# Performance work log

Hardware: AMD Instinct MI355X
Metric: run time of the kernel (lower is better)

The kernel has to match this reference:

```python
import jax, jax.numpy as jnp
import numpy as np

T, B, V, H = 128, 32, 10000, 1024

def setup_inputs() -> dict:
    key = jax.random.key(0)
    ks = jax.random.split(key, 9)
    inp = {
        "inputs": jax.random.normal(ks[0], (T, B, V), dtype=jnp.float32),
        "H0": jnp.zeros((B, H), dtype=jnp.float32),
        "W_xz": jax.random.normal(ks[1], (V, H), dtype=jnp.float32) * 0.01,
        "W_hz": jax.random.normal(ks[2], (H, H), dtype=jnp.float32) * 0.01,
        "b_z": jnp.zeros((H,), dtype=jnp.float32),
        "W_xr": jax.random.normal(ks[3], (V, H), dtype=jnp.float32) * 0.01,
        "W_hr": jax.random.normal(ks[4], (H, H), dtype=jnp.float32) * 0.01,
        "b_r": jnp.zeros((H,), dtype=jnp.float32),
        "W_xh": jax.random.normal(ks[5], (V, H), dtype=jnp.float32) * 0.01,
        "W_hh": jax.random.normal(ks[6], (H, H), dtype=jnp.float32) * 0.01,
        "b_h": jnp.zeros((H,), dtype=jnp.float32),
        "W_hq": jax.random.normal(ks[7], (H, V), dtype=jnp.float32) * 0.01,
        "b_q": jnp.zeros((V,), dtype=jnp.float32),
    }
    return inp


def reference(inputs, H0, W_xz, W_hz, b_z, W_xr, W_hr, b_r, W_xh, W_hh, b_h, W_hq, b_q):
    # Batch all input-side projections across the whole sequence (same math,
    # just hoisted out of the recurrence): [T,B,V] @ [V,H] -> [T,B,H]
    Xz = jnp.einsum('tbv,vh->tbh', inputs, W_xz) + b_z
    Xr = jnp.einsum('tbv,vh->tbh', inputs, W_xr) + b_r
    Xh = jnp.einsum('tbv,vh->tbh', inputs, W_xh) + b_h

    def step(Hprev, xs):
        xz, xr, xh = xs
        Z = jax.nn.sigmoid(xz + Hprev @ W_hz)
        R = jax.nn.sigmoid(xr + Hprev @ W_hr)
        H_tilda = jnp.tanh(xh + (R * Hprev) @ W_hh)
        Hn = Z * Hprev + (1.0 - Z) * H_tilda
        return Hn, Hn

    H_last, Hs = jax.lax.scan(step, H0, (Xz, Xr, Xh))  # Hs: [T,B,H]
    outputs = jnp.einsum('tbh,hv->tbv', Hs, W_hq) + b_q  # [T,B,V]
    return outputs, H_last
```

## Files before the change

kernel.cpp:

```cpp
#include <hip/hip_runtime.h>
#include <cstdint>

typedef unsigned short u16;
typedef __attribute__((ext_vector_type(8))) short bf16x8;
typedef __attribute__((ext_vector_type(4))) float f32x4;
typedef __attribute__((ext_vector_type(4))) unsigned short u16x4;

#define AS_GLOBAL __attribute__((address_space(1)))
#define AS_LDS    __attribute__((address_space(3)))

__device__ __forceinline__ void gld_lds16(const void* g, void* l) {
    __builtin_amdgcn_global_load_lds((const AS_GLOBAL unsigned int*)g,
                                     (AS_LDS unsigned int*)l, 16, 0, 0);
}

__device__ __forceinline__ u16 f2bf(float f) {
    union { float f; unsigned int u; } v; v.f = f;
    unsigned int u = v.u;
    u = (u + 0x7FFFu + ((u >> 16) & 1u)) >> 16;
    return (u16)u;
}

__device__ __forceinline__ f32x4 mfma16(bf16x8 a, bf16x8 b, f32x4 c) {
    return __builtin_amdgcn_mfma_f32_16x16x32_bf16(a, b, c, 0, 0, 0);
}

__device__ __forceinline__ float sigm(float x) {
    return 1.f / (1.f + __expf(-x));
}

__global__ __launch_bounds__(256) void gemm_bt(
    const u16* __restrict__ A, const u16* __restrict__ BT,
    const float* __restrict__ bias, float* __restrict__ C,
    int M, int N, int K, int ldc, int Nstore)
{
    __shared__ u16 As[128 * 32];
    __shared__ u16 Bs[128 * 32];

    const int tid  = threadIdx.x;
    const int lane = tid & 63;
    const int wave = tid >> 6;
    const int quad = lane >> 4;
    const int l16  = lane & 15;
    const int m0 = blockIdx.y * 128;
    const int n0 = blockIdx.x * 128;
    const int wm = (wave >> 1) * 64;
    const int wn = (wave & 1) * 64;

    f32x4 acc[4][4];
#pragma unroll
    for (int i = 0; i < 4; i++)
#pragma unroll
        for (int j = 0; j < 4; j++) acc[i][j] = (f32x4){0.f, 0.f, 0.f, 0.f};

    const int s0 = tid, s1 = tid + 256;
    const int r0 = s0 >> 2, c0 = (s0 & 3) * 8;
    const int r1 = s1 >> 2, c1 = (s1 & 3) * 8;

    const u16* ga0 = A  + (size_t)(m0 + r0) * K + c0;
    const u16* ga1 = A  + (size_t)(m0 + r1) * K + c1;
    const u16* gb0 = BT + (size_t)(n0 + r0) * K + c0;
    const u16* gb1 = BT + (size_t)(n0 + r1) * K + c1;
    u16* la0 = &As[s0 * 8];
    u16* la1 = &As[s1 * 8];
    u16* lb0 = &Bs[s0 * 8];
    u16* lb1 = &Bs[s1 * 8];

    const u16* lra = &As[(wm + l16) * 32 + quad * 8];
    const u16* lrb = &Bs[(wn + l16) * 32 + quad * 8];

    const int nk = K >> 5;
    for (int kb = 0; kb < nk; ++kb) {
        const int k0 = kb << 5;
        gld_lds16(ga0 + k0, la0);
        gld_lds16(ga1 + k0, la1);
        gld_lds16(gb0 + k0, lb0);
        gld_lds16(gb1 + k0, lb1);
        __syncthreads();
        bf16x8 a[4], b[4];
#pragma unroll
        for (int i = 0; i < 4; i++) a[i] = *(const bf16x8*)(lra + i * 16 * 32);
#pragma unroll
        for (int j = 0; j < 4; j++) b[j] = *(const bf16x8*)(lrb + j * 16 * 32);
#pragma unroll
        for (int i = 0; i < 4; i++)
#pragma unroll
            for (int j = 0; j < 4; j++)
                acc[i][j] = mfma16(a[i], b[j], acc[i][j]);
        __syncthreads();
    }

#pragma unroll
    for (int i = 0; i < 4; i++) {
#pragma unroll
        for (int r = 0; r < 4; r++) {
            const int row = m0 + wm + i * 16 + quad * 4 + r;
#pragma unroll
            for (int j = 0; j < 4; j++) {
                const int col = n0 + wn + j * 16 + l16;
                if (col < Nstore)
                    C[(size_t)row * ldc + col] = acc[i][j][r] + bias[col];
            }
        }
    }
}

__global__ __launch_bounds__(256) void k_step1(
    const u16* __restrict__ Hbf, const float* __restrict__ Hf,
    const float* __restrict__ Xzr,
    const u16* __restrict__ WzrT,
    float* __restrict__ Zbuf, u16* __restrict__ RHbf)
{
    const int tid = threadIdx.x, lane = tid & 63, wave = tid >> 6;
    const int quad = lane >> 4, l16 = lane & 15;
    const int n0 = (blockIdx.x * 4 + wave) * 16;

    f32x4 acc0 = (f32x4){0,0,0,0}, acc1 = (f32x4){0,0,0,0};
    const u16* Arow0 = Hbf + l16 * 1024 + quad * 8;
    const u16* Arow1 = Hbf + (16 + l16) * 1024 + quad * 8;
    const u16* Brow  = WzrT + (size_t)(n0 + l16) * 1024 + quad * 8;
#pragma unroll 8
    for (int kb = 0; kb < 32; ++kb) {
        bf16x8 a0 = *(const bf16x8*)(Arow0 + kb * 32);
        bf16x8 a1 = *(const bf16x8*)(Arow1 + kb * 32);
        bf16x8 b  = *(const bf16x8*)(Brow + kb * 32);
        acc0 = mfma16(a0, b, acc0);
        acc1 = mfma16(a1, b, acc1);
    }
    const int n = n0 + l16;
#pragma unroll
    for (int r = 0; r < 4; r++) {
        const int b0 = quad * 4 + r;
        const int b1 = b0 + 16;
        float v0 = acc0[r] + Xzr[b0 * 3072 + n];
        float v1 = acc1[r] + Xzr[b1 * 3072 + n];
        if (n < 1024) {
            Zbuf[b0 * 1024 + n] = sigm(v0);
            Zbuf[b1 * 1024 + n] = sigm(v1);
        } else {
            const int m_ = n - 1024;
            RHbf[b0 * 1024 + m_] = f2bf(sigm(v0) * Hf[b0 * 1024 + m_]);
            RHbf[b1 * 1024 + m_] = f2bf(sigm(v1) * Hf[b1 * 1024 + m_]);
        }
    }
}

__global__ __launch_bounds__(256) void k_step2(
    const u16* __restrict__ RHbf, const u16* __restrict__ WhhT,
    const float* __restrict__ Xh,
    const float* __restrict__ Zbuf,
    float* __restrict__ Hf, u16* __restrict__ Hbf, u16* __restrict__ Hsbf_t)
{
    const int tid = threadIdx.x, lane = tid & 63, wave = tid >> 6;
    const int quad = lane >> 4, l16 = lane & 15;
    const int n0 = (blockIdx.x * 4 + wave) * 16;

    f32x4 acc0 = (f32x4){0,0,0,0}, acc1 = (f32x4){0,0,0,0};
    const u16* Arow0 = RHbf + l16 * 1024 + quad * 8;
    const u16* Arow1 = RHbf + (16 + l16) * 1024 + quad * 8;
    const u16* Brow  = WhhT + (size_t)(n0 + l16) * 1024 + quad * 8;
#pragma unroll 8
    for (int kb = 0; kb < 32; ++kb) {
        bf16x8 a0 = *(const bf16x8*)(Arow0 + kb * 32);
        bf16x8 a1 = *(const bf16x8*)(Arow1 + kb * 32);
        bf16x8 b  = *(const bf16x8*)(Brow + kb * 32);
        acc0 = mfma16(a0, b, acc0);
        acc1 = mfma16(a1, b, acc1);
    }
    const int n = n0 + l16;
#pragma unroll
    for (int r = 0; r < 4; r++) {
        const int b0 = quad * 4 + r;
        const int b1 = b0 + 16;
#pragma unroll
        for (int s = 0; s < 2; s++) {
            const int bb = s ? b1 : b0;
            float v = (s ? acc1[r] : acc0[r]) + Xh[bb * 3072 + n];
            float ht = tanhf(v);
            float z  = Zbuf[bb * 1024 + n];
            float hp = Hf[bb * 1024 + n];
            float hn = z * hp + (1.f - z) * ht;
            Hf[bb * 1024 + n] = hn;
            u16 hb = f2bf(hn);
            Hbf[bb * 1024 + n] = hb;
            Hsbf_t[bb * 1024 + n] = hb;
        }
    }
}

__global__ void k_cast_pad(const float* __restrict__ src, u16* __restrict__ dst,
                           int rows, int K0, int Kp)
{
    const size_t total = (size_t)rows * (size_t)(Kp >> 2);
    for (size_t idx = (size_t)blockIdx.x * blockDim.x + threadIdx.x;
         idx < total; idx += (size_t)gridDim.x * blockDim.x) {
        const int kq = (int)(idx % (size_t)(Kp >> 2));
        const int r  = (int)(idx / (size_t)(Kp >> 2));
        const int k  = kq << 2;
        u16x4 o;
        if (k + 3 < K0) {
            const float4 v = *(const float4*)(src + (size_t)r * K0 + k);
            o[0] = f2bf(v.x); o[1] = f2bf(v.y); o[2] = f2bf(v.z); o[3] = f2bf(v.w);
        } else {
#pragma unroll
            for (int i = 0; i < 4; i++)
                o[i] = (k + i < K0) ? f2bf(src[(size_t)r * K0 + k + i]) : (u16)0;
        }
        *(u16x4*)(dst + (size_t)r * Kp + k) = o;
    }
}

__global__ void k_transpose_cast(const float* __restrict__ src, u16* __restrict__ dst,
                                 int K0, int N0, int Kp, int rowOff)
{
    __shared__ float tile[32][33];
    const int kb = blockIdx.x * 32, nb = blockIdx.y * 32;
    const int tx = threadIdx.x, ty = threadIdx.y;
#pragma unroll
    for (int i = 0; i < 4; i++) {
        const int k = kb + ty + i * 8, n = nb + tx;
        tile[ty + i * 8][tx] = (k < K0 && n < N0) ? src[(size_t)k * N0 + n] : 0.f;
    }
    __syncthreads();
#pragma unroll
    for (int i = 0; i < 4; i++) {
        const int n = nb + ty + i * 8, k = kb + tx;
        dst[(size_t)(rowOff + n) * Kp + k] = f2bf(tile[tx][ty + i * 8]);
    }
}

__global__ void k_bias_cat(const float* __restrict__ bz, const float* __restrict__ br,
                           const float* __restrict__ bh, float* __restrict__ bcat)
{
    const int i = blockIdx.x * 256 + threadIdx.x;
    if (i < 1024) bcat[i] = bz[i];
    else if (i < 2048) bcat[i] = br[i - 1024];
    else if (i < 3072) bcat[i] = bh[i - 2048];
}

__global__ void k_h0(const float* __restrict__ H0, float* __restrict__ Hf,
                     u16* __restrict__ Hbf)
{
    const int i = blockIdx.x * 256 + threadIdx.x;
    if (i < 32 * 1024) { float v = H0[i]; Hf[i] = v; Hbf[i] = f2bf(v); }
}

extern "C" void kernel_launch(void* const* d_in, const int* in_sizes, int n_in,
                              void* d_out, int out_size, void* d_ws, size_t ws_size,
                              hipStream_t stream)
{
    const float* inputs = (const float*)d_in[0];
    const float* H0     = (const float*)d_in[1];
    const float* W_xz   = (const float*)d_in[2];
    const float* W_hz   = (const float*)d_in[3];
    const float* b_z    = (const float*)d_in[4];
    const float* W_xr   = (const float*)d_in[5];
    const float* W_hr   = (const float*)d_in[6];
    const float* b_r    = (const float*)d_in[7];
    const float* W_xh   = (const float*)d_in[8];
    const float* W_hh   = (const float*)d_in[9];
    const float* b_h    = (const float*)d_in[10];
    const float* W_hq   = (const float*)d_in[11];
    const float* b_q    = (const float*)d_in[12];
    float* out = (float*)d_out;

    constexpr int T = 128, B = 32, V = 10000, H = 1024;
    constexpr int Vp = 10016;
    constexpr int MB = T * B;
    constexpr int Np3 = 10112;

    char* p = (char*)d_ws;
    auto alloc = [&](size_t bytes) -> void* {
        void* q = (void*)p; p += (bytes + 255) & ~(size_t)255; return q;
    };
    u16*   Abf  = (u16*)  alloc((size_t)MB * Vp * 2);
    u16*   WxT  = (u16*)  alloc((size_t)3072 * Vp * 2);
    float* Xzrh = (float*)alloc((size_t)MB * 3072 * 4);
    u16*   Hsbf = (u16*)  alloc((size_t)MB * H * 2);
    u16*   WzrT = (u16*)  alloc((size_t)2048 * H * 2);
    u16*   WhhT = (u16*)  alloc((size_t)H * H * 2);
    u16*   WhqT = (u16*)  alloc((size_t)Np3 * H * 2);
    float* bcat = (float*)alloc(3072 * 4);
    float* Hf   = (float*)alloc((size_t)B * H * 4);
    u16*   Hbf  = (u16*)  alloc((size_t)B * H * 2);
    float* Zbuf = (float*)alloc((size_t)B * H * 4);
    u16*   RHbf = (u16*)  alloc((size_t)B * H * 2);

    {
        size_t total = (size_t)MB * (Vp / 4);
        int blocks = (int)((total + 255) / 256);
        k_cast_pad<<<blocks, 256, 0, stream>>>(inputs, Abf, MB, V, Vp);
    }
    dim3 tb(32, 8);
    k_transpose_cast<<<dim3(Vp / 32, H / 32), tb, 0, stream>>>(W_xz, WxT, V, H, Vp, 0);
    k_transpose_cast<<<dim3(Vp / 32, H / 32), tb, 0, stream>>>(W_xr, WxT, V, H, Vp, 1024);
    k_transpose_cast<<<dim3(Vp / 32, H / 32), tb, 0, stream>>>(W_xh, WxT, V, H, Vp, 2048);
    k_transpose_cast<<<dim3(H / 32, H / 32), tb, 0, stream>>>(W_hz, WzrT, H, H, H, 0);
    k_transpose_cast<<<dim3(H / 32, H / 32), tb, 0, stream>>>(W_hr, WzrT, H, H, H, 1024);
    k_transpose_cast<<<dim3(H / 32, H / 32), tb, 0, stream>>>(W_hh, WhhT, H, H, H, 0);
    k_transpose_cast<<<dim3(H / 32, Np3 / 32), tb, 0, stream>>>(W_hq, WhqT, H, V, H, 0);
    k_bias_cat<<<12, 256, 0, stream>>>(b_z, b_r, b_h, bcat);
    k_h0<<<128, 256, 0, stream>>>(H0, Hf, Hbf);

    gemm_bt<<<dim3(3072 / 128, MB / 128), 256, 0, stream>>>(
        Abf, WxT, bcat, Xzrh, MB, 3072, Vp, 3072, 3072);

    for (int t = 0; t < T; ++t) {
        k_step1<<<32, 256, 0, stream>>>(
            Hbf, Hf, Xzrh + (size_t)t * B * 3072, WzrT, Zbuf, RHbf);
        k_step2<<<16, 256, 0, stream>>>(
            RHbf, WhhT, Xzrh + (size_t)t * B * 3072 + 2048, Zbuf,
            Hf, Hbf, Hsbf + (size_t)t * B * H);
    }

    gemm_bt<<<dim3(Np3 / 128, MB / 128), 256, 0, stream>>>(
        Hsbf, WhqT, b_q, out, MB, Np3, H, V, V);

    hipMemcpyAsync(out + (size_t)MB * V, Hf, (size_t)B * H * 4,
                   hipMemcpyDeviceToDevice, stream);
}
```

Measured before the change: 4.999 ms.

## Fuse recurrence steps into one persistent cooperative kernel with LDS-resident weights

Replaces the 256 per-timestep kernel launches with a single cooperative kernel that loops over all timesteps, separating the gate phase and the candidate phase with grid-wide barriers. Each block loads its slice of the recurrent weight matrices into LDS once and reuses it across every step, avoiding repeated global/L2 weight reads. The second GEMM splits K across waves with an LDS reduction. The cost is two grid syncs per step, occupancy limited by the large LDS footprint, and reliance on cooperative launch residency.

New measurement: 4.482 ms. 10.3% less time.

```diff
diff --git a/kernel.cpp b/kernel.cpp
--- a/kernel.cpp
+++ b/kernel.cpp
@@ -1,5 +1,8 @@
 #include <hip/hip_runtime.h>
+#include <hip/hip_cooperative_groups.h>
 #include <cstdint>
+
+namespace cg = cooperative_groups;
 
 typedef unsigned short u16;
 typedef __attribute__((ext_vector_type(8))) short bf16x8;
@@ -105,86 +108,112 @@
     }
 }
 
-__global__ __launch_bounds__(256) void k_step1(
-    const u16* __restrict__ Hbf, const float* __restrict__ Hf,
-    const float* __restrict__ Xzr,
+#define WPAD 1032
+
+__global__ __launch_bounds__(256) void k_recurrence(
     const u16* __restrict__ WzrT,
-    float* __restrict__ Zbuf, u16* __restrict__ RHbf)
-{
-    const int tid = threadIdx.x, lane = tid & 63, wave = tid >> 6;
-    const int quad = lane >> 4, l16 = lane & 15;
-    const int n0 = (blockIdx.x * 4 + wave) * 16;
-
-    f32x4 acc0 = (f32x4){0,0,0,0}, acc1 = (f32x4){0,0,0,0};
-    const u16* Arow0 = Hbf + l16 * 1024 + quad * 8;
-    const u16* Arow1 = Hbf + (16 + l16) * 1024 + quad * 8;
-    const u16* Brow  = WzrT + (size_t)(n0 + l16) * 1024 + quad * 8;
+    const u16* __restrict__ WhhT,
+    const float* __restrict__ Xzrh,
+    float* __restrict__ Hf,
+    u16* __restrict__ Hbf,
+    float* __restrict__ Zbuf,
+    u16* __restrict__ RHbf,
+    u16* __restrict__ Hsbf,
+    int T)
+{
+    __shared__ __align__(16) u16 Wzr_s[32 * WPAD];
+    __shared__ __align__(16) u16 Whh_s[16 * WPAD];
+    __shared__ __align__(16) float red[2][64][4];
+
+    const int tid  = threadIdx.x;
+    const int lane = tid & 63;
+    const int wave = tid >> 6;
+    const int quad = lane >> 4;
+    const int l16  = lane & 15;
+    const int blk  = blockIdx.x;
+
+    for (int i = tid; i < 32 * 128; i += 256) {
+        const int r = i >> 7, c = (i & 127) * 8;
+        *(bf16x8*)(&Wzr_s[r * WPAD + c]) =
+            *(const bf16x8*)(WzrT + (size_t)(blk * 32 + r) * 1024 + c);
+    }
+    for (int i = tid; i < 16 * 128; i += 256) {
+        const int r = i >> 7, c = (i & 127) * 8;
+        *(bf16x8*)(&Whh_s[r * WPAD + c]) =
+            *(const bf16x8*)(WhhT + (size_t)(blk * 16 + r) * 1024 + c);
+    }
+    __syncthreads();
+
+    cg::grid_group grid = cg::this_grid();
+
+    for (int t = 0; t < T; ++t) {
+        const float* Xzr = Xzrh + (size_t)t * 32 * 3072;
+
+        {
+            const int tn = wave & 1;
+            const int mt = wave >> 1;
+            const int ng = blk * 32 + tn * 16 + l16;
+            const u16* Arow = Hbf + (mt * 16 + l16) * 1024 + quad * 8;
+            const u16* Brow = &Wzr_s[(tn * 16 + l16) * WPAD + quad * 8];
+            f32x4 acc = (f32x4){0,0,0,0}, acc2 = (f32x4){0,0,0,0};
 #pragma unroll 8
-    for (int kb = 0; kb < 32; ++kb) {
-        bf16x8 a0 = *(const bf16x8*)(Arow0 + kb * 32);
-        bf16x8 a1 = *(const bf16x8*)(Arow1 + kb * 32);
-        bf16x8 b  = *(const bf16x8*)(Brow + kb * 32);
-        acc0 = mfma16(a0, b, acc0);
-        acc1 = mfma16(a1, b, acc1);
-    }
-    const int n = n0 + l16;
-#pragma unroll
-    for (int r = 0; r < 4; r++) {
-        const int b0 = quad * 4 + r;
-        const int b1 = b0 + 16;
-        float v0 = acc0[r] + Xzr[b0 * 3072 + n];
-        float v1 = acc1[r] + Xzr[b1 * 3072 + n];
-        if (n < 1024) {
-            Zbuf[b0 * 1024 + n] = sigm(v0);
-            Zbuf[b1 * 1024 + n] = sigm(v1);
-        } else {
-            const int m_ = n - 1024;
-            RHbf[b0 * 1024 + m_] = f2bf(sigm(v0) * Hf[b0 * 1024 + m_]);
-            RHbf[b1 * 1024 + m_] = f2bf(sigm(v1) * Hf[b1 * 1024 + m_]);
+            for (int kb = 0; kb < 32; kb += 2) {
+                acc  = mfma16(*(const bf16x8*)(Arow + kb * 32),
+                              *(const bf16x8*)(Brow + kb * 32), acc);
+                acc2 = mfma16(*(const bf16x8*)(Arow + kb * 32 + 32),
+                              *(const bf16x8*)(Brow + kb * 32 + 32), acc2);
+            }
+            acc += acc2;
+#pragma unroll
+            for (int r = 0; r < 4; r++) {
+                const int row = mt * 16 + quad * 4 + r;
+                const float v = acc[r] + Xzr[row * 3072 + ng];
+                if (ng < 1024) {
+                    Zbuf[row * 1024 + ng] = sigm(v);
+                } else {
+                    const int m_ = ng - 1024;
+                    RHbf[row * 1024 + m_] = f2bf(sigm(v) * Hf[row * 1024 + m_]);
+                }
+            }
         }
-    }
-}
-
-__global__ __launch_bounds__(256) void k_step2(
-    const u16* __restrict__ RHbf, const u16* __restrict__ WhhT,
-    const float* __restrict__ Xh,
-    const float* __restrict__ Zbuf,
-    float* __restrict__ Hf, u16* __restrict__ Hbf, u16* __restrict__ Hsbf_t)
-{
-    const int tid = threadIdx.x, lane = tid & 63, wave = tid >> 6;
-    const int quad = lane >> 4, l16 = lane & 15;
-    const int n0 = (blockIdx.x * 4 + wave) * 16;
-
-    f32x4 acc0 = (f32x4){0,0,0,0}, acc1 = (f32x4){0,0,0,0};
-    const u16* Arow0 = RHbf + l16 * 1024 + quad * 8;
-    const u16* Arow1 = RHbf + (16 + l16) * 1024 + quad * 8;
-    const u16* Brow  = WhhT + (size_t)(n0 + l16) * 1024 + quad * 8;
+        grid.sync();
+
+        {
+            const int mt = wave & 1;
+            const int kh = wave >> 1;
+            const int n  = blk * 16 + l16;
+            const u16* Arow = RHbf + (mt * 16 + l16) * 1024 + kh * 512 + quad * 8;
+            const u16* Brow = &Whh_s[l16 * WPAD + kh * 512 + quad * 8];
+            f32x4 acc = (f32x4){0,0,0,0}, acc2 = (f32x4){0,0,0,0};
 #pragma unroll 8
-    for (int kb = 0; kb < 32; ++kb) {
-        bf16x8 a0 = *(const bf16x8*)(Arow0 + kb * 32);
-        bf16x8 a1 = *(const bf16x8*)(Arow1 + kb * 32);
-        bf16x8 b  = *(const bf16x8*)(Brow + kb * 32);
-        acc0 = mfma16(a0, b, acc0);
-        acc1 = mfma16(a1, b, acc1);
-    }
-    const int n = n0 + l16;
-#pragma unroll
-    for (int r = 0; r < 4; r++) {
-        const int b0 = quad * 4 + r;
-        const int b1 = b0 + 16;
-#pragma unroll
-        for (int s = 0; s < 2; s++) {
-            const int bb = s ? b1 : b0;
-            float v = (s ? acc1[r] : acc0[r]) + Xh[bb * 3072 + n];
-            float ht = tanhf(v);
-            float z  = Zbuf[bb * 1024 + n];
-            float hp = Hf[bb * 1024 + n];
-            float hn = z * hp + (1.f - z) * ht;
-            Hf[bb * 1024 + n] = hn;
-            u16 hb = f2bf(hn);
-            Hbf[bb * 1024 + n] = hb;
-            Hsbf_t[bb * 1024 + n] = hb;
+            for (int kb = 0; kb < 16; kb += 2) {
+                acc  = mfma16(*(const bf16x8*)(Arow + kb * 32),
+                              *(const bf16x8*)(Brow + kb * 32), acc);
+                acc2 = mfma16(*(const bf16x8*)(Arow + kb * 32 + 32),
+                              *(const bf16x8*)(Brow + kb * 32 + 32), acc2);
+            }
+            acc += acc2;
+            if (kh == 1) *(f32x4*)(&red[mt][lane][0]) = acc;
+            __syncthreads();
+            if (kh == 0) {
+                acc += *(const f32x4*)(&red[mt][lane][0]);
+                u16* Hs_t = Hsbf + (size_t)t * 32 * 1024;
+#pragma unroll
+                for (int r = 0; r < 4; r++) {
+                    const int row = mt * 16 + quad * 4 + r;
+                    const float v  = acc[r] + Xzr[row * 3072 + 2048 + n];
+                    const float ht = tanhf(v);
+                    const float z  = Zbuf[row * 1024 + n];
+                    const float hp = Hf[row * 1024 + n];
+                    const float hn = z * hp + (1.f - z) * ht;
+                    Hf[row * 1024 + n] = hn;
+                    const u16 hb = f2bf(hn);
+                    Hbf[row * 1024 + n]  = hb;
+                    Hs_t[row * 1024 + n] = hb;
+                }
+            }
         }
+        grid.sync();
     }
 }
 
@@ -305,12 +334,13 @@
     gemm_bt<<<dim3(3072 / 128, MB / 128), 256, 0, stream>>>(
         Abf, WxT, bcat, Xzrh, MB, 3072, Vp, 3072, 3072);
 
-    for (int t = 0; t < T; ++t) {
-        k_step1<<<32, 256, 0, stream>>>(
-            Hbf, Hf, Xzrh + (size_t)t * B * 3072, WzrT, Zbuf, RHbf);
-        k_step2<<<16, 256, 0, stream>>>(
-            RHbf, WhhT, Xzrh + (size_t)t * B * 3072 + 2048, Zbuf,
-            Hf, Hbf, Hsbf + (size_t)t * B * H);
+    {
+        int Tloc = T;
+        void* kargs[] = { (void*)&WzrT, (void*)&WhhT, (void*)&Xzrh, (void*)&Hf,
+                          (void*)&Hbf, (void*)&Zbuf, (void*)&RHbf, (void*)&Hsbf,
+                          (void*)&Tloc };
+        hipLaunchCooperativeKernel((const void*)k_recurrence, dim3(64), dim3(256),
+                                   kargs, 0, stream);
     }
 
     gemm_bt<<<dim3(Np3 / 128, MB / 128), 256, 0, stream>>>(
```
